# Kernel optimization log

Hardware: AMD Instinct MI355X
Metric: run time of the kernel (lower is better)

Reference implementation:

```python
import jax, jax.numpy as jnp
import numpy as np


def setup_inputs() -> dict:
    key = jax.random.key(0)
    k1, k2, k3, k4, k5 = jax.random.split(key, 5)
    B, S, D, H, E = 4, 4096, 1024, 1024, 8  # H = per-expert hidden (fuel_dim)
    std = 0.02
    return {
        "hidden_states": jax.random.normal(k1, (B, S, D), dtype=jnp.float32),
        "gate_w": jax.random.normal(k2, (D, E), dtype=jnp.float32) * std,
        "gw": jax.random.normal(k3, (E, D, H), dtype=jnp.float32) * std,
        "pw": jax.random.normal(k4, (E, D, H), dtype=jnp.float32) * std,
        "ow": jax.random.normal(k5, (E, H, D), dtype=jnp.float32) * std,
        "top_k": 2,
    }


def reference(hidden_states, gate_w, gw, pw, ow, top_k):
    B, S, D = hidden_states.shape
    E = gate_w.shape[1]
    x = hidden_states.reshape(-1, D)  # [T, D]
    T = x.shape[0]

    # Router
    router_logits = x @ gate_w  # [T, E]
    routing_probs = jax.nn.softmax(router_logits.astype(jnp.float32), axis=-1)
    top_w, top_i = jax.lax.top_k(routing_probs, top_k)  # [T, k]
    top_w = top_w / jnp.sum(top_w, axis=-1, keepdims=True)
    top_w = top_w.astype(x.dtype)

    # Dense combine weights: zero for unselected experts -> same math as
    # the torch gather/expert/scatter loop.
    combine = jnp.zeros((T, E), dtype=x.dtype).at[
        jnp.arange(T)[:, None], top_i
    ].set(top_w)  # [T, E]

    # SwiGLU experts, batched over the expert dim.
    g = jnp.einsum('td,edh->eth', x, gw)          # [E, T, H]
    p = jnp.einsum('td,edh->eth', x, pw)          # [E, T, H]
    h = g * jax.nn.silu(p)                        # [E, T, H]
    y = jnp.einsum('eth,ehd->etd', h, ow)         # [E, T, D]
    final = jnp.einsum('etd,te->td', y, combine)  # [T, D]
    final = final.reshape(B, S, D)

    # Load-balancing loss (recomputes softmax/topk as the torch fn does)
    expert_mask = jax.nn.one_hot(top_i, E, dtype=jnp.float32)  # [T, k, E]
    tokens_per_expert = jnp.mean(expert_mask, axis=0)          # [k, E]
    router_prob_per_expert = jnp.mean(routing_probs, axis=0)   # [E]
    bl_loss = jnp.sum(tokens_per_expert * router_prob_per_expert[None, :]) * E

    return final, router_logits, bl_loss
```

## Files before the change

### kernel.cpp

```cpp
#include <hip/hip_runtime.h>
#include <hip/hip_bf16.h>
#include <cstdint>

#define T_TOK 16384
#define DDIM  1024
#define HDIM  1024
#define NEXP  8

typedef __attribute__((ext_vector_type(8))) short bf16x8;
typedef __attribute__((ext_vector_type(4))) float f32x4;

__device__ __forceinline__ unsigned short f2bf(float f) {
  unsigned u = __builtin_bit_cast(unsigned, f);
  return (unsigned short)((u + 0x7fffu + ((u >> 16) & 1u)) >> 16);
}
__device__ __forceinline__ unsigned pk2(float a, float b) {
  return (unsigned)f2bf(a) | ((unsigned)f2bf(b) << 16);
}

__global__ __launch_bounds__(256) void convert_k(
    const float* __restrict__ gw, const float* __restrict__ pw,
    const float* __restrict__ ow, char* __restrict__ wg,
    char* __restrict__ wp, char* __restrict__ wo) {
  __shared__ float t[64][65];
  const int z = blockIdx.z;
  const int arr = z >> 3, e = z & 7;
  const float* src = (arr == 0 ? gw : arr == 1 ? pw : ow) + ((long)e << 20);
  char* dst = (arr == 0 ? wg : arr == 1 ? wp : wo) + ((long)e << 21);
  const int r0 = blockIdx.x * 64, c0 = blockIdx.y * 64;
  const int row = threadIdx.x >> 2, q = threadIdx.x & 3;
  const float4* sp = (const float4*)(src + (long)(r0 + row) * 1024 + c0 + q * 16);
  float4 v0 = sp[0], v1 = sp[1], v2 = sp[2], v3 = sp[3];
  float* tr = &t[row][q * 16];
  tr[0]=v0.x; tr[1]=v0.y; tr[2]=v0.z; tr[3]=v0.w;
  tr[4]=v1.x; tr[5]=v1.y; tr[6]=v1.z; tr[7]=v1.w;
  tr[8]=v2.x; tr[9]=v2.y; tr[10]=v2.z; tr[11]=v2.w;
  tr[12]=v3.x; tr[13]=v3.y; tr[14]=v3.z; tr[15]=v3.w;
  __syncthreads();
  const int cl = row, rq = q;
  uint4 o0, o1;
  o0.x = pk2(t[rq*16+ 0][cl], t[rq*16+ 1][cl]);
  o0.y = pk2(t[rq*16+ 2][cl], t[rq*16+ 3][cl]);
  o0.z = pk2(t[rq*16+ 4][cl], t[rq*16+ 5][cl]);
  o0.w = pk2(t[rq*16+ 6][cl], t[rq*16+ 7][cl]);
  o1.x = pk2(t[rq*16+ 8][cl], t[rq*16+ 9][cl]);
  o1.y = pk2(t[rq*16+10][cl], t[rq*16+11][cl]);
  o1.z = pk2(t[rq*16+12][cl], t[rq*16+13][cl]);
  o1.w = pk2(t[rq*16+14][cl], t[rq*16+15][cl]);
  char* dp = dst + (long)(c0 + cl) * 2048 + (long)(r0 + rq * 16) * 2;
  *(uint4*)dp = o0;
  *(uint4*)(dp + 16) = o1;
}

__global__ __launch_bounds__(256) void router_k(
    const float* __restrict__ x, const float* __restrict__ gatew,
    float* __restrict__ logitsOut, float4* __restrict__ route,
    float* __restrict__ accum) {
  __shared__ float accB[16];
  const int tid = threadIdx.x;
  if (tid < 16) accB[tid] = 0.f;
  __syncthreads();
  const int lane = tid & 63;
  const int gwave = blockIdx.x * 4 + (tid >> 6);

  for (int g = gwave; g < 4096; g += 1024) {
    const int t0 = g * 4;
    float s[4][8];
#pragma unroll
    for (int tt = 0; tt < 4; ++tt)
#pragma unroll
      for (int e = 0; e < 8; ++e) s[tt][e] = 0.f;

    for (int i = 0; i < 16; ++i) {
      int d = lane + i * 64;
      float4 w0 = *(const float4*)(gatew + d * 8);
      float4 w1 = *(const float4*)(gatew + d * 8 + 4);
#pragma unroll
      for (int tt = 0; tt < 4; ++tt) {
        float xv = x[(long)(t0 + tt) * DDIM + d];
        s[tt][0] += xv * w0.x; s[tt][1] += xv * w0.y;
        s[tt][2] += xv * w0.z; s[tt][3] += xv * w0.w;
        s[tt][4] += xv * w1.x; s[tt][5] += xv * w1.y;
        s[tt][6] += xv * w1.z; s[tt][7] += xv * w1.w;
      }
    }
#pragma unroll
    for (int m = 1; m < 64; m <<= 1)
#pragma unroll
      for (int tt = 0; tt < 4; ++tt)
#pragma unroll
        for (int e = 0; e < 8; ++e) s[tt][e] += __shfl_xor(s[tt][e], m);

    float psum[8];
#pragma unroll
    for (int e = 0; e < 8; ++e) psum[e] = 0.f;
    int i1a[4], i2a[4];
    float w1a[4], w2a[4];
#pragma unroll
    for (int tt = 0; tt < 4; ++tt) {
      float mx = s[tt][0];
#pragma unroll
      for (int e = 1; e < 8; ++e) mx = fmaxf(mx, s[tt][e]);
      float pe[8], Z = 0.f;
#pragma unroll
      for (int e = 0; e < 8; ++e) { pe[e] = __expf(s[tt][e] - mx); Z += pe[e]; }
      float inv = 1.f / Z;
#pragma unroll
      for (int e = 0; e < 8; ++e) { pe[e] *= inv; psum[e] += pe[e]; }
      int i1 = 0; float p1 = pe[0];
#pragma unroll
      for (int e = 1; e < 8; ++e) if (pe[e] > p1) { p1 = pe[e]; i1 = e; }
      int i2 = -1; float p2 = -1.f;
#pragma unroll
      for (int e = 0; e < 8; ++e)
        if (e != i1 && pe[e] > p2) { p2 = pe[e]; i2 = e; }
      float wsum = p1 + p2;
      i1a[tt] = i1; i2a[tt] = i2;
      w1a[tt] = p1 / wsum; w2a[tt] = p2 / wsum;
    }
    if (lane < 32) {
      int tt = lane >> 3, e = lane & 7;
      logitsOut[(t0 + tt) * 8 + e] = s[tt][e];
    }
    if (lane < 32 && (lane & 7) == 0) {
      int tt = lane >> 3;
      float4 rr;
      rr.x = w1a[tt]; rr.y = w2a[tt];
      rr.z = __int_as_float(i1a[tt]); rr.w = __int_as_float(i2a[tt]);
      route[t0 + tt] = rr;
    }
    if (lane < 8) {
      float c = 0.f;
#pragma unroll
      for (int tt = 0; tt < 4; ++tt)
        c += (float)(i1a[tt] == lane) + (float)(i2a[tt] == lane);
      atomicAdd(&accB[lane], psum[lane]);
      atomicAdd(&accB[8 + lane], c);
    }
  }
  __syncthreads();
  if (tid < 16) atomicAdd(&accum[tid], accB[tid]);
}

__global__ void offsets_k(const float* __restrict__ accum,
                          int* __restrict__ offs, int* __restrict__ cursor) {
  if (threadIdx.x == 0) {
    int c = 0;
#pragma unroll
    for (int e = 0; e < 8; ++e) {
      offs[e] = c; cursor[e] = c;
      c += (int)(accum[8 + e] + 0.5f);
    }
    offs[8] = c;
  }
}

__global__ __launch_bounds__(256) void scatter_k(
    const float4* __restrict__ route, int* __restrict__ cursor,
    int* __restrict__ list, float* __restrict__ wsl) {
  int t = blockIdx.x * 256 + threadIdx.x;
  float4 rr = route[t];
  int i1 = __float_as_int(rr.z), i2 = __float_as_int(rr.w);
  int s1 = atomicAdd(&cursor[i1], 1);
  list[s1] = t; wsl[s1] = rr.x;
  int s2 = atomicAdd(&cursor[i2], 1);
  list[s2] = t; wsl[s2] = rr.y;
}

__global__ __launch_bounds__(512) void pass1_k(
    const float* __restrict__ x, const char* __restrict__ wg,
    const char* __restrict__ wp, const int* __restrict__ list,
    const float* __restrict__ wsl, const int* __restrict__ offs,
    char* __restrict__ hw) {
  __shared__ __align__(16) char Al[16384];
  __shared__ __align__(16) char Bg[16384];
  __shared__ __align__(16) char Bp[16384];
  const int e = blockIdx.x >> 7, tile = blockIdx.x & 127;
  const int s0 = offs[e], s1 = offs[e + 1];
  const int start = s0 + tile * 128;
  if (start >= s1) return;
  const int valid = min(128, s1 - start);
  const int chunk = blockIdx.y;
  const int tid = threadIdx.x;
  const int lane = tid & 63, wid = tid >> 6;

  const int sr = tid >> 2, q = tid & 3;
  const int tokA = list[start + min(sr, valid - 1)];
  const float* axp = x + (long)tokA * DDIM + q * 16;
  const unsigned swz = ((unsigned)(sr & 7)) << 4;
  const unsigned sb = (unsigned)(sr * 128 + q * 32);
  const long bbase = ((long)e << 21) + ((long)(chunk * 128 + sr) << 11) + q * 32;

  f32x4 aG[4][2], aP[4][2];
#pragma unroll
  for (int f = 0; f < 4; ++f)
#pragma unroll
    for (int j = 0; j < 2; ++j) {
      aG[f][j] = (f32x4){0.f, 0.f, 0.f, 0.f};
      aP[f][j] = (f32x4){0.f, 0.f, 0.f, 0.f};
    }

  const int col = lane & 15, kg = lane >> 4;
  const int mb = (wid >> 2) * 64, nb = (wid & 3) * 32;

  for (int ks16 = 0; ks16 < 16; ++ks16) {
    const int k0 = ks16 * 64;
    __syncthreads();
    {
      const float4* ap = (const float4*)(axp + k0);
      float4 v0 = ap[0], v1 = ap[1], v2 = ap[2], v3 = ap[3];
      uint4 w0, w1;
      w0.x = pk2(v0.x, v0.y); w0.y = pk2(v0.z, v0.w);
      w0.z = pk2(v1.x, v1.y); w0.w = pk2(v1.z, v1.w);
      w1.x = pk2(v2.x, v2.y); w1.y = pk2(v2.z, v2.w);
      w1.z = pk2(v3.x, v3.y); w1.w = pk2(v3.z, v3.w);
      *(uint4*)(Al + (sb ^ swz)) = w0;
      *(uint4*)(Al + ((sb + 16) ^ swz)) = w1;
      const uint4* gp = (const uint4*)(wg + bbase + (k0 << 1));
      uint4 g0 = gp[0], g1 = gp[1];
      const uint4* pp = (const uint4*)(wp + bbase + (k0 << 1));
      uint4 p0 = pp[0], p1 = pp[1];
      *(uint4*)(Bg + (sb ^ swz)) = g0;
      *(uint4*)(Bg + ((sb + 16) ^ swz)) = g1;
      *(uint4*)(Bp + (sb ^ swz)) = p0;
      *(uint4*)(Bp + ((sb + 16) ^ swz)) = p1;
    }
    __syncthreads();
#pragma unroll
    for (int ks = 0; ks < 2; ++ks) {
      bf16x8 af[4], bg2[2], bp2[2];
#pragma unroll
      for (int f = 0; f < 4; ++f) {
        int r = mb + f * 16 + col;
        af[f] = *(const bf16x8*)(
            Al + ((unsigned)(r * 128 + ks * 64 + kg * 16) ^
                  (((unsigned)r & 7u) << 4)));
      }
#pragma unroll
      for (int j = 0; j < 2; ++j) {
        int n = nb + j * 16 + col;
        unsigned off = (unsigned)(n * 128 + ks * 64 + kg * 16) ^
                       (((unsigned)n & 7u) << 4);
        bg2[j] = *(const bf16x8*)(Bg + off);
        bp2[j] = *(const bf16x8*)(Bp + off);
      }
#pragma unroll
      for (int f = 0; f < 4; ++f)
#pragma unroll
        for (int j = 0; j < 2; ++j) {
          aG[f][j] = __builtin_amdgcn_mfma_f32_16x16x32_bf16(af[f], bg2[j],
                                                             aG[f][j], 0, 0, 0);
          aP[f][j] = __builtin_amdgcn_mfma_f32_16x16x32_bf16(af[f], bp2[j],
                                                             aP[f][j], 0, 0, 0);
        }
    }
  }
  const int rg = lane >> 4;
#pragma unroll
  for (int f = 0; f < 4; ++f) {
#pragma unroll
    for (int r = 0; r < 4; ++r) {
      int ml = mb + f * 16 + rg * 4 + r;
      if (ml < valid) {
        int slot = start + ml;
        float wv = wsl[slot];
#pragma unroll
        for (int j = 0; j < 2; ++j) {
          float g = aG[f][j][r], p = aP[f][j][r];
          float h = g * (p / (1.f + __expf(-p))) * wv;
          int hc = chunk * 128 + nb + j * 16 + col;
          *(unsigned short*)(hw + (((long)slot << 11) + (hc << 1))) = f2bf(h);
        }
      }
    }
  }
}

__global__ __launch_bounds__(512) void pass2_k(
    const char* __restrict__ hw, const char* __restrict__ wo,
    const int* __restrict__ list, const int* __restrict__ offs,
    float* __restrict__ out) {
  __shared__ __align__(16) char Al[16384];
  __shared__ __align__(16) char Bl[32768];
  const int e = blockIdx.x >> 7, tile = blockIdx.x & 127;
  const int s0 = offs[e], s1 = offs[e + 1];
  const int start = s0 + tile * 128;
  if (start >= s1) return;
  const int valid = min(128, s1 - start);
  const int chunk = blockIdx.y;
  const int tid = threadIdx.x;
  const int lane = tid & 63, wid = tid >> 6;

  const int ar = tid >> 2, aq = tid & 3;
  const long asrc = ((long)(start + min(ar, valid - 1)) << 11) + aq * 32;
  const unsigned awz = ((unsigned)(ar & 7)) << 4;
  const unsigned ab = (unsigned)(ar * 128 + aq * 32);
  const int bn = tid >> 1, bq = tid & 1;
  const long bsrc = ((long)e << 21) + ((long)(chunk * 256 + bn) << 11) + bq * 64;
  const unsigned bwz = ((unsigned)(bn & 7)) << 4;
  const unsigned bb = (unsigned)(bn * 128 + bq * 64);

  f32x4 acc[4][4];
#pragma unroll
  for (int f = 0; f < 4; ++f)
#pragma unroll
    for (int j = 0; j < 4; ++j) acc[f][j] = (f32x4){0.f, 0.f, 0.f, 0.f};

  const int col = lane & 15, kg = lane >> 4;
  const int mb = (wid >> 2) * 64, nb = (wid & 3) * 64;

  for (int ks16 = 0; ks16 < 16; ++ks16) {
    const int k0b = ks16 * 128;
    __syncthreads();
    {
      const uint4* ap = (const uint4*)(hw + asrc + k0b);
      uint4 a0 = ap[0], a1 = ap[1];
      *(uint4*)(Al + (ab ^ awz)) = a0;
      *(uint4*)(Al + ((ab + 16) ^ awz)) = a1;
      const uint4* bp = (const uint4*)(wo + bsrc + k0b);
      uint4 b0 = bp[0], b1 = bp[1], b2 = bp[2], b3 = bp[3];
      *(uint4*)(Bl + (bb ^ bwz)) = b0;
      *(uint4*)(Bl + ((bb + 16) ^ bwz)) = b1;
      *(uint4*)(Bl + ((bb + 32) ^ bwz)) = b2;
      *(uint4*)(Bl + ((bb + 48) ^ bwz)) = b3;
    }
    __syncthreads();
#pragma unroll
    for (int ks = 0; ks < 2; ++ks) {
      bf16x8 af[4], bf4[4];
#pragma unroll
      for (int f = 0; f < 4; ++f) {
        int r = mb + f * 16 + col;
        af[f] = *(const bf16x8*)(
            Al + ((unsigned)(r * 128 + ks * 64 + kg * 16) ^
                  (((unsigned)r & 7u) << 4)));
      }
#pragma unroll
      for (int j = 0; j < 4; ++j) {
        int n = nb + j * 16 + col;
        bf4[j] = *(const bf16x8*)(
            Bl + ((unsigned)(n * 128 + ks * 64 + kg * 16) ^
                  (((unsigned)n & 7u) << 4)));
      }
#pragma unroll
      for (int f = 0; f < 4; ++f)
#pragma unroll
        for (int j = 0; j < 4; ++j)
          acc[f][j] = __builtin_amdgcn_mfma_f32_16x16x32_bf16(af[f], bf4[j],
                                                              acc[f][j], 0, 0, 0);
    }
  }
  const int rg = lane >> 4;
#pragma unroll
  for (int f = 0; f < 4; ++f) {
#pragma unroll
    for (int r = 0; r < 4; ++r) {
      int ml = mb + f * 16 + rg * 4 + r;
      if (ml < valid) {
        int token = list[start + ml];
#pragma unroll
        for (int j = 0; j < 4; ++j) {
          int c = chunk * 256 + nb + j * 16 + col;
          atomicAdd(&out[(long)token * DDIM + c], acc[f][j][r]);
        }
      }
    }
  }
}

__global__ void loss_k(const float* __restrict__ accum, float* __restrict__ out) {
  if (threadIdx.x == 0 && blockIdx.x == 0) {
    float L = 0.f;
#pragma unroll
    for (int e = 0; e < 8; ++e) L += accum[e] * accum[8 + e];
    out[0] = L * 8.f / ((float)T_TOK * (float)T_TOK);
  }
}

extern "C" void kernel_launch(void* const* d_in, const int* in_sizes, int n_in,
                              void* d_out, int out_size, void* d_ws,
                              size_t ws_size, hipStream_t stream) {
  const float* x     = (const float*)d_in[0];
  const float* gatew = (const float*)d_in[1];
  const float* gw    = (const float*)d_in[2];
  const float* pw    = (const float*)d_in[3];
  const float* ow    = (const float*)d_in[4];

  float* out       = (float*)d_out;
  float* logitsOut = out + (long)T_TOK * DDIM;
  float* lossOut   = out + (long)T_TOK * DDIM + T_TOK * 8;

  char* wsB = (char*)d_ws;
  float*  accum  = (float*)wsB;
  int*    cursor = (int*)(wsB + 64);
  int*    offs   = (int*)(wsB + 96);
  float4* route  = (float4*)(wsB + 1024);
  int*    list   = (int*)(wsB + 263168);
  float*  wsl    = (float*)(wsB + 394240);
  char*   wg     = wsB + (1l << 20);
  char*   wp     = wsB + 17825792;
  char*   wo     = wsB + 34603008;
  char*   hw     = wsB + 51380224;

  hipMemsetAsync(d_out, 0, (size_t)out_size * 4, stream);
  hipMemsetAsync(accum, 0, 64, stream);
  convert_k<<<dim3(16, 16, 24), 256, 0, stream>>>(gw, pw, ow, wg, wp, wo);
  router_k<<<256, 256, 0, stream>>>(x, gatew, logitsOut, route, accum);
  offsets_k<<<1, 64, 0, stream>>>(accum, offs, cursor);
  scatter_k<<<64, 256, 0, stream>>>(route, cursor, list, wsl);
  pass1_k<<<dim3(1024, 8), 512, 0, stream>>>(x, wg, wp, list, wsl, offs, hw);
  pass2_k<<<dim3(1024, 4), 512, 0, stream>>>(hw, wo, list, offs, out);
  loss_k<<<1, 64, 0, stream>>>(accum, lossOut);
}
```

Before: 615.5 us.

## Double-buffer MoE GEMM tiles with async global-to-LDS loads and bf16 x copy

```diff
diff --git a/kernel.cpp b/kernel.cpp
--- a/kernel.cpp
+++ b/kernel.cpp
@@ -4,8 +4,6 @@
 
 #define T_TOK 16384
 #define DDIM  1024
-#define HDIM  1024
-#define NEXP  8
 
 typedef __attribute__((ext_vector_type(8))) short bf16x8;
 typedef __attribute__((ext_vector_type(4))) float f32x4;
@@ -16,6 +14,11 @@
 }
 __device__ __forceinline__ unsigned pk2(float a, float b) {
   return (unsigned)f2bf(a) | ((unsigned)f2bf(b) << 16);
+}
+__device__ __forceinline__ void gload16(const void* g, void* l) {
+  typedef __attribute__((address_space(1))) const unsigned int gu32;
+  typedef __attribute__((address_space(3))) unsigned int lu32;
+  __builtin_amdgcn_global_load_lds((gu32*)g, (lu32*)l, 16, 0, 0);
 }
 
 __global__ __launch_bounds__(256) void convert_k(
@@ -55,7 +58,7 @@
 __global__ __launch_bounds__(256) void router_k(
     const float* __restrict__ x, const float* __restrict__ gatew,
     float* __restrict__ logitsOut, float4* __restrict__ route,
-    float* __restrict__ accum) {
+    float* __restrict__ accum, unsigned short* __restrict__ xbo) {
   __shared__ float accB[16];
   const int tid = threadIdx.x;
   if (tid < 16) accB[tid] = 0.f;
@@ -78,6 +81,7 @@
 #pragma unroll
       for (int tt = 0; tt < 4; ++tt) {
         float xv = x[(long)(t0 + tt) * DDIM + d];
+        if (xbo) xbo[(long)(t0 + tt) * DDIM + d] = f2bf(xv);
         s[tt][0] += xv * w0.x; s[tt][1] += xv * w0.y;
         s[tt][2] += xv * w0.z; s[tt][3] += xv * w0.w;
         s[tt][4] += xv * w1.x; s[tt][5] += xv * w1.y;
@@ -167,29 +171,42 @@
   list[s2] = t; wsl[s2] = rr.y;
 }
 
+template <int XB>
 __global__ __launch_bounds__(512) void pass1_k(
-    const float* __restrict__ x, const char* __restrict__ wg,
-    const char* __restrict__ wp, const int* __restrict__ list,
-    const float* __restrict__ wsl, const int* __restrict__ offs,
-    char* __restrict__ hw) {
-  __shared__ __align__(16) char Al[16384];
-  __shared__ __align__(16) char Bg[16384];
-  __shared__ __align__(16) char Bp[16384];
+    const float* __restrict__ x, const unsigned short* __restrict__ xb,
+    const char* __restrict__ wg, const char* __restrict__ wp,
+    const int* __restrict__ list, const float* __restrict__ wsl,
+    const int* __restrict__ offs, char* __restrict__ hw) {
+  __shared__ __align__(16) char Al[2][16384];
+  __shared__ __align__(16) char Bgl[2][16384];
+  __shared__ __align__(16) char Bpl[2][16384];
   const int e = blockIdx.x >> 7, tile = blockIdx.x & 127;
   const int s0 = offs[e], s1 = offs[e + 1];
   const int start = s0 + tile * 128;
   if (start >= s1) return;
   const int valid = min(128, s1 - start);
   const int chunk = blockIdx.y;
-  const int tid = threadIdx.x;
-  const int lane = tid & 63, wid = tid >> 6;
-
+  const int tid = threadIdx.x, lane = tid & 63, wid = tid >> 6;
+
+  const int l8 = lane >> 3, seg = lane & 7;
+  const unsigned inrow = ((unsigned)(seg * 16)) ^ (((unsigned)l8) << 4);
+  const int br0 = wid * 16 + l8, br1 = br0 + 8;
+  const long wbase = ((long)e << 21) + ((long)(chunk * 128) << 11);
+  const char* gsrc0 = wg + wbase + ((long)br0 << 11) + inrow;
+  const char* gsrc1 = wg + wbase + ((long)br1 << 11) + inrow;
+  const char* psrc0 = wp + wbase + ((long)br0 << 11) + inrow;
+  const char* psrc1 = wp + wbase + ((long)br1 << 11) + inrow;
+  const unsigned ld0 = (unsigned)(wid * 2048), ld1 = ld0 + 1024;
+
+  const int tokA0 = list[start + min(br0, valid - 1)];
+  const int tokA1 = list[start + min(br1, valid - 1)];
+  const char* asrc0 = (const char*)xb + ((long)tokA0 << 11) + inrow;
+  const char* asrc1 = (const char*)xb + ((long)tokA1 << 11) + inrow;
   const int sr = tid >> 2, q = tid & 3;
-  const int tokA = list[start + min(sr, valid - 1)];
-  const float* axp = x + (long)tokA * DDIM + q * 16;
+  const int tokS = list[start + min(sr, valid - 1)];
+  const float* axp = x + (long)tokS * DDIM + q * 16;
   const unsigned swz = ((unsigned)(sr & 7)) << 4;
   const unsigned sb = (unsigned)(sr * 128 + q * 32);
-  const long bbase = ((long)e << 21) + ((long)(chunk * 128 + sr) << 11) + q * 32;
 
   f32x4 aG[4][2], aP[4][2];
 #pragma unroll
@@ -203,58 +220,76 @@
   const int col = lane & 15, kg = lane >> 4;
   const int mb = (wid >> 2) * 64, nb = (wid & 3) * 32;
 
-  for (int ks16 = 0; ks16 < 16; ++ks16) {
-    const int k0 = ks16 * 64;
-    __syncthreads();
-    {
-      const float4* ap = (const float4*)(axp + k0);
-      float4 v0 = ap[0], v1 = ap[1], v2 = ap[2], v3 = ap[3];
-      uint4 w0, w1;
-      w0.x = pk2(v0.x, v0.y); w0.y = pk2(v0.z, v0.w);
-      w0.z = pk2(v1.x, v1.y); w0.w = pk2(v1.z, v1.w);
-      w1.x = pk2(v2.x, v2.y); w1.y = pk2(v2.z, v2.w);
-      w1.z = pk2(v3.x, v3.y); w1.w = pk2(v3.z, v3.w);
-      *(uint4*)(Al + (sb ^ swz)) = w0;
-      *(uint4*)(Al + ((sb + 16) ^ swz)) = w1;
-      const uint4* gp = (const uint4*)(wg + bbase + (k0 << 1));
-      uint4 g0 = gp[0], g1 = gp[1];
-      const uint4* pp = (const uint4*)(wp + bbase + (k0 << 1));
-      uint4 p0 = pp[0], p1 = pp[1];
-      *(uint4*)(Bg + (sb ^ swz)) = g0;
-      *(uint4*)(Bg + ((sb + 16) ^ swz)) = g1;
-      *(uint4*)(Bp + (sb ^ swz)) = p0;
-      *(uint4*)(Bp + ((sb + 16) ^ swz)) = p1;
-    }
-    __syncthreads();
+#define P1_STAGE_B(kb, buf)                                   \
+  {                                                           \
+    long ko = (long)(kb) << 7;                                \
+    gload16(gsrc0 + ko, &Bgl[buf][ld0]);                      \
+    gload16(gsrc1 + ko, &Bgl[buf][ld1]);                      \
+    gload16(psrc0 + ko, &Bpl[buf][ld0]);                      \
+    gload16(psrc1 + ko, &Bpl[buf][ld1]);                      \
+  }
+#define P1_STAGE_A_XB(kb, buf)                                \
+  {                                                           \
+    long ko = (long)(kb) << 7;                                \
+    gload16(asrc0 + ko, &Al[buf][ld0]);                       \
+    gload16(asrc1 + ko, &Al[buf][ld1]);                       \
+  }
+#define P1_STAGE_A_F32(kb, buf)                               \
+  {                                                           \
+    const float4* ap = (const float4*)(axp + (kb) * 64);      \
+    float4 v0 = ap[0], v1 = ap[1], v2 = ap[2], v3 = ap[3];    \
+    uint4 w0, w1;                                             \
+    w0.x = pk2(v0.x, v0.y); w0.y = pk2(v0.z, v0.w);           \
+    w0.z = pk2(v1.x, v1.y); w0.w = pk2(v1.z, v1.w);           \
+    w1.x = pk2(v2.x, v2.y); w1.y = pk2(v2.z, v2.w);           \
+    w1.z = pk2(v3.x, v3.y); w1.w = pk2(v3.z, v3.w);           \
+    *(uint4*)(&Al[buf][0] + (sb ^ swz)) = w0;                 \
+    *(uint4*)(&Al[buf][0] + ((sb + 16) ^ swz)) = w1;          \
+  }
+
+  if (XB) P1_STAGE_A_XB(0, 0) else P1_STAGE_A_F32(0, 0);
+  P1_STAGE_B(0, 0);
+  __syncthreads();
+
+  for (int kb = 0; kb < 16; ++kb) {
+    const int cur = kb & 1;
+    bf16x8 af[2][4], bg2[2][2], bp2[2][2];
 #pragma unroll
     for (int ks = 0; ks < 2; ++ks) {
-      bf16x8 af[4], bg2[2], bp2[2];
 #pragma unroll
       for (int f = 0; f < 4; ++f) {
         int r = mb + f * 16 + col;
-        af[f] = *(const bf16x8*)(
-            Al + ((unsigned)(r * 128 + ks * 64 + kg * 16) ^
-                  (((unsigned)r & 7u) << 4)));
+        af[ks][f] = *(const bf16x8*)(
+            &Al[cur][0] + ((unsigned)(r * 128 + ks * 64 + kg * 16) ^
+                           (((unsigned)r & 7u) << 4)));
       }
 #pragma unroll
       for (int j = 0; j < 2; ++j) {
         int n = nb + j * 16 + col;
         unsigned off = (unsigned)(n * 128 + ks * 64 + kg * 16) ^
                        (((unsigned)n & 7u) << 4);
-        bg2[j] = *(const bf16x8*)(Bg + off);
-        bp2[j] = *(const bf16x8*)(Bp + off);
-      }
+        bg2[ks][j] = *(const bf16x8*)(&Bgl[cur][0] + off);
+        bp2[ks][j] = *(const bf16x8*)(&Bpl[cur][0] + off);
+      }
+    }
+    if (kb < 15) {
+      if (XB) P1_STAGE_A_XB(kb + 1, cur ^ 1) else P1_STAGE_A_F32(kb + 1, cur ^ 1);
+      P1_STAGE_B(kb + 1, cur ^ 1);
+    }
+#pragma unroll
+    for (int ks = 0; ks < 2; ++ks)
 #pragma unroll
       for (int f = 0; f < 4; ++f)
 #pragma unroll
         for (int j = 0; j < 2; ++j) {
-          aG[f][j] = __builtin_amdgcn_mfma_f32_16x16x32_bf16(af[f], bg2[j],
-                                                             aG[f][j], 0, 0, 0);
-          aP[f][j] = __builtin_amdgcn_mfma_f32_16x16x32_bf16(af[f], bp2[j],
-                                                             aP[f][j], 0, 0, 0);
+          aG[f][j] = __builtin_amdgcn_mfma_f32_16x16x32_bf16(
+              af[ks][f], bg2[ks][j], aG[f][j], 0, 0, 0);
+          aP[f][j] = __builtin_amdgcn_mfma_f32_16x16x32_bf16(
+              af[ks][f], bp2[ks][j], aP[f][j], 0, 0, 0);
         }
-    }
-  }
+    __syncthreads();
+  }
+
   const int rg = lane >> 4;
 #pragma unroll
   for (int f = 0; f < 4; ++f) {
@@ -280,25 +315,31 @@
     const char* __restrict__ hw, const char* __restrict__ wo,
     const int* __restrict__ list, const int* __restrict__ offs,
     float* __restrict__ out) {
-  __shared__ __align__(16) char Al[16384];
-  __shared__ __align__(16) char Bl[32768];
+  __shared__ __align__(16) char Al[2][16384];
+  __shared__ __align__(16) char Bl[2][32768];
   const int e = blockIdx.x >> 7, tile = blockIdx.x & 127;
   const int s0 = offs[e], s1 = offs[e + 1];
   const int start = s0 + tile * 128;
   if (start >= s1) return;
   const int valid = min(128, s1 - start);
   const int chunk = blockIdx.y;
-  const int tid = threadIdx.x;
-  const int lane = tid & 63, wid = tid >> 6;
-
-  const int ar = tid >> 2, aq = tid & 3;
-  const long asrc = ((long)(start + min(ar, valid - 1)) << 11) + aq * 32;
-  const unsigned awz = ((unsigned)(ar & 7)) << 4;
-  const unsigned ab = (unsigned)(ar * 128 + aq * 32);
-  const int bn = tid >> 1, bq = tid & 1;
-  const long bsrc = ((long)e << 21) + ((long)(chunk * 256 + bn) << 11) + bq * 64;
-  const unsigned bwz = ((unsigned)(bn & 7)) << 4;
-  const unsigned bb = (unsigned)(bn * 128 + bq * 64);
+  const int tid = threadIdx.x, lane = tid & 63, wid = tid >> 6;
+
+  const int l8 = lane >> 3, seg = lane & 7;
+  const unsigned inrow = ((unsigned)(seg * 16)) ^ (((unsigned)l8) << 4);
+  const int ar0 = wid * 16 + l8, ar1 = ar0 + 8;
+  const char* asrc0 = hw + ((long)(start + min(ar0, valid - 1)) << 11) + inrow;
+  const char* asrc1 = hw + ((long)(start + min(ar1, valid - 1)) << 11) + inrow;
+  const unsigned lda0 = (unsigned)(wid * 2048), lda1 = lda0 + 1024;
+  const long wobase = ((long)e << 21) + ((long)(chunk * 256) << 11);
+  const char* bsrc[4];
+  unsigned ldb[4];
+#pragma unroll
+  for (int i = 0; i < 4; ++i) {
+    int n = wid * 32 + i * 8 + l8;
+    bsrc[i] = wo + wobase + ((long)n << 11) + inrow;
+    ldb[i] = (unsigned)(wid * 4096 + i * 1024);
+  }
 
   f32x4 acc[4][4];
 #pragma unroll
@@ -309,47 +350,52 @@
   const int col = lane & 15, kg = lane >> 4;
   const int mb = (wid >> 2) * 64, nb = (wid & 3) * 64;
 
-  for (int ks16 = 0; ks16 < 16; ++ks16) {
-    const int k0b = ks16 * 128;
-    __syncthreads();
-    {
-      const uint4* ap = (const uint4*)(hw + asrc + k0b);
-      uint4 a0 = ap[0], a1 = ap[1];
-      *(uint4*)(Al + (ab ^ awz)) = a0;
-      *(uint4*)(Al + ((ab + 16) ^ awz)) = a1;
-      const uint4* bp = (const uint4*)(wo + bsrc + k0b);
-      uint4 b0 = bp[0], b1 = bp[1], b2 = bp[2], b3 = bp[3];
-      *(uint4*)(Bl + (bb ^ bwz)) = b0;
-      *(uint4*)(Bl + ((bb + 16) ^ bwz)) = b1;
-      *(uint4*)(Bl + ((bb + 32) ^ bwz)) = b2;
-      *(uint4*)(Bl + ((bb + 48) ^ bwz)) = b3;
-    }
-    __syncthreads();
+#define P2_STAGE(kb, buf)                                     \
+  {                                                           \
+    long ko = (long)(kb) << 7;                                \
+    gload16(asrc0 + ko, &Al[buf][lda0]);                      \
+    gload16(asrc1 + ko, &Al[buf][lda1]);                      \
+    gload16(bsrc[0] + ko, &Bl[buf][ldb[0]]);                  \
+    gload16(bsrc[1] + ko, &Bl[buf][ldb[1]]);                  \
+    gload16(bsrc[2] + ko, &Bl[buf][ldb[2]]);                  \
+    gload16(bsrc[3] + ko, &Bl[buf][ldb[3]]);                  \
+  }
+
+  P2_STAGE(0, 0);
+  __syncthreads();
+
+  for (int kb = 0; kb < 16; ++kb) {
+    const int cur = kb & 1;
+    bf16x8 af[2][4], bf4[2][4];
 #pragma unroll
     for (int ks = 0; ks < 2; ++ks) {
-      bf16x8 af[4], bf4[4];
 #pragma unroll
       for (int f = 0; f < 4; ++f) {
         int r = mb + f * 16 + col;
-        af[f] = *(const bf16x8*)(
-            Al + ((unsigned)(r * 128 + ks * 64 + kg * 16) ^
-                  (((unsigned)r & 7u) << 4)));
+        af[ks][f] = *(const bf16x8*)(
+            &Al[cur][0] + ((unsigned)(r * 128 + ks * 64 + kg * 16) ^
+                           (((unsigned)r & 7u) << 4)));
       }
 #pragma unroll
       for (int j = 0; j < 4; ++j) {
         int n = nb + j * 16 + col;
-        bf4[j] = *(const bf16x8*)(
-            Bl + ((unsigned)(n * 128 + ks * 64 + kg * 16) ^
-                  (((unsigned)n & 7u) << 4)));
-      }
+        bf4[ks][j] = *(const bf16x8*)(
+            &Bl[cur][0] + ((unsigned)(n * 128 + ks * 64 + kg * 16) ^
+                           (((unsigned)n & 7u) << 4)));
+      }
+    }
+    if (kb < 15) P2_STAGE(kb + 1, cur ^ 1);
+#pragma unroll
+    for (int ks = 0; ks < 2; ++ks)
 #pragma unroll
       for (int f = 0; f < 4; ++f)
 #pragma unroll
         for (int j = 0; j < 4; ++j)
-          acc[f][j] = __builtin_amdgcn_mfma_f32_16x16x32_bf16(af[f], bf4[j],
-                                                              acc[f][j], 0, 0, 0);
-    }
-  }
+          acc[f][j] = __builtin_amdgcn_mfma_f32_16x16x32_bf16(
+              af[ks][f], bf4[ks][j], acc[f][j], 0, 0, 0);
+    __syncthreads();
+  }
+
   const int rg = lane >> 4;
 #pragma unroll
   for (int f = 0; f < 4; ++f) {
@@ -401,14 +447,22 @@
   char*   wp     = wsB + 17825792;
   char*   wo     = wsB + 34603008;
   char*   hw     = wsB + 51380224;
+  unsigned short* xb = (unsigned short*)(wsB + 118489088);
+  const bool big = ws_size >= 152043520ul;
 
   hipMemsetAsync(d_out, 0, (size_t)out_size * 4, stream);
   hipMemsetAsync(accum, 0, 64, stream);
   convert_k<<<dim3(16, 16, 24), 256, 0, stream>>>(gw, pw, ow, wg, wp, wo);
-  router_k<<<256, 256, 0, stream>>>(x, gatew, logitsOut, route, accum);
+  router_k<<<256, 256, 0, stream>>>(x, gatew, logitsOut, route, accum,
+                                    big ? xb : nullptr);
   offsets_k<<<1, 64, 0, stream>>>(accum, offs, cursor);
   scatter_k<<<64, 256, 0, stream>>>(route, cursor, list, wsl);
-  pass1_k<<<dim3(1024, 8), 512, 0, stream>>>(x, wg, wp, list, wsl, offs, hw);
+  if (big)
+    pass1_k<1><<<dim3(1024, 8), 512, 0, stream>>>(x, xb, wg, wp, list, wsl,
+                                                  offs, hw);
+  else
+    pass1_k<0><<<dim3(1024, 8), 512, 0, stream>>>(x, xb, wg, wp, list, wsl,
+                                                  offs, hw);
   pass2_k<<<dim3(1024, 4), 512, 0, stream>>>(hw, wo, list, offs, out);
   loss_k<<<1, 64, 0, stream>>>(accum, lossOut);
 }
```

New measurement: 737.9 us. 1.2x slower.
